# Optimization experiments

Hardware: AMD Instinct MI355X
Metric: run time of the kernel (lower is better)

Reference implementation:

```python
import jax, jax.numpy as jnp
import numpy as np

# dims: 3 bert layers averaged, B batch, T_SUB subword tokens (excl. CLS), W words, D=768 bert dim
B, T_SUB, W, D = 64, 512, 256, 768
H = 20          # lstm_hidden
CAP_DIM = 10
CAP_TYPES = 4
IN_DIM = D + CAP_DIM


def setup_inputs() -> dict:
    key = jax.random.key(0)
    ks = jax.random.split(key, 10)
    hiddens = jax.random.normal(ks[0], (3, B, T_SUB + 1, D), jnp.float32)  # [CLS] at pos 0
    # nondecreasing word ids, each word gets exactly T_SUB//W subwords (all segments non-empty)
    bert2toks = jnp.tile(jnp.repeat(jnp.arange(W), T_SUB // W)[None, :], (B, 1)).astype(jnp.int32)
    cap_inds = jax.random.randint(ks[1], (B, W), 0, CAP_TYPES)
    cap_table = jax.random.normal(ks[2], (CAP_TYPES, CAP_DIM), jnp.float32) * 0.1
    s = 1.0 / np.sqrt(H)
    u = lambda k, shp: jax.random.uniform(k, shp, jnp.float32, -s, s)
    w_ih_f = u(ks[3], (4 * H, IN_DIM))
    w_hh_f = u(ks[4], (4 * H, H))
    b_f = u(ks[5], (4 * H,))  # b_ih + b_hh fused
    w_ih_b = u(ks[6], (4 * H, IN_DIM))
    w_hh_b = u(ks[7], (4 * H, H))
    b_b = u(ks[8], (4 * H,))
    return {"hiddens": hiddens, "bert2toks": bert2toks, "cap_inds": cap_inds,
            "cap_table": cap_table, "w_ih_f": w_ih_f, "w_hh_f": w_hh_f, "b_f": b_f,
            "w_ih_b": w_ih_b, "w_hh_b": w_hh_b, "b_b": b_b}


def _lstm_dir(xs, w_ih, w_hh, b, reverse):
    # xs: [B, W, IN_DIM] -> hs: [B, W, H]
    xs_t = jnp.swapaxes(xs, 0, 1)  # [W, B, IN]
    if reverse:
        xs_t = xs_t[::-1]
    h0 = jnp.zeros((xs.shape[0], H), xs.dtype)

    def step(carry, xt):
        h, c = carry
        g = xt @ w_ih.T + h @ w_hh.T + b  # [B, 4H], pytorch gate order i,f,g,o
        i, f, gg, o = jnp.split(g, 4, axis=-1)
        c = jax.nn.sigmoid(f) * c + jax.nn.sigmoid(i) * jnp.tanh(gg)
        h = jax.nn.sigmoid(o) * jnp.tanh(c)
        return (h, c), h

    _, hs = jax.lax.scan(step, (h0, h0), xs_t)
    if reverse:
        hs = hs[::-1]
    return jnp.swapaxes(hs, 0, 1)


def reference(hiddens, bert2toks, cap_inds, cap_table,
              w_ih_f, w_hh_f, b_f, w_ih_b, w_hh_b, b_b):
    # mean over the 3 selected bert layers
    means = jnp.mean(hiddens, axis=0)          # [B, T_SUB+1, D]
    sub = means[:, 1:T_SUB + 1]                # skip [CLS]: means[i+1] indexing
    # ragged subword->word mean pooling as a segment mean
    flat_ids = (bert2toks + jnp.arange(B, dtype=bert2toks.dtype)[:, None] * W).reshape(-1)
    sums = jax.ops.segment_sum(sub.reshape(B * T_SUB, D), flat_ids, num_segments=B * W)
    cnts = jax.ops.segment_sum(jnp.ones((B * T_SUB, 1), sub.dtype), flat_ids, num_segments=B * W)
    word_h = (sums / cnts).reshape(B, W, D)
    cap_emb = cap_table[cap_inds]              # [B, W, CAP_DIM]
    x = jnp.concatenate([word_h, cap_emb], axis=-1)  # [B, W, IN_DIM]
    out = jnp.concatenate([
        _lstm_dir(x, w_ih_f, w_hh_f, b_f, False),
        _lstm_dir(x, w_ih_b, w_hh_b, b_b, True),
    ], axis=-1)                                # [B, W, 2H]
    return out
```

## Files before the change

kernel.cpp:

```cpp
#include <hip/hip_runtime.h>
#include <math.h>

#define BB 64
#define T_SUB 512
#define WW 256
#define DD 768
#define HH 20
#define CAP_DIM 10
#define IN_DIM 778
#define KPAD 800
#define G4 80
#define NOUT 160

typedef _Float16 f16x8 __attribute__((ext_vector_type(8)));
typedef float f32x4 __attribute__((ext_vector_type(4)));
typedef unsigned int uint2v __attribute__((ext_vector_type(2)));

#define WP_OFF   ((size_t)0)
#define SEG_OFF  ((size_t)256000)
#define X_OFF    ((size_t)387072)

__global__ __launch_bounds__(256) void k_prep(
    const float* __restrict__ wf, const float* __restrict__ wb,
    const int* __restrict__ b2t,
    _Float16* __restrict__ wp, int2* __restrict__ seg)
{
    int blk = blockIdx.x;
    if (blk < NOUT) {
        int j = blk;
        const float* src = (j < G4) ? (wf + (size_t)j * IN_DIM)
                                    : (wb + (size_t)(j - G4) * IN_DIM);
        for (int k = threadIdx.x; k < KPAD; k += 256)
            wp[(size_t)j * KPAD + k] = (k < IN_DIM) ? (_Float16)src[k] : (_Float16)0.f;
    } else {
        int b = blk - NOUT, w = threadIdx.x;
        const int* row = b2t + (size_t)b * T_SUB;
        int lo = 0, hi = T_SUB;
        while (lo < hi) { int m = (lo + hi) >> 1; if (row[m] < w) lo = m + 1; else hi = m; }
        int lo2 = lo, hi2 = T_SUB;
        while (lo2 < hi2) { int m = (lo2 + hi2) >> 1; if (row[m] < w + 1) lo2 = m + 1; else hi2 = m; }
        seg[(size_t)b * WW + w] = make_int2(lo, lo2 - lo);
    }
}

__global__ __launch_bounds__(256) void k_mean(
    const float* __restrict__ hiddens, const int2* __restrict__ seg,
    const int* __restrict__ cap_inds, const float* __restrict__ cap_table,
    _Float16* __restrict__ x)
{
    int idx = blockIdx.x * 256 + threadIdx.x;
    int d8 = idx % 100;
    int bw = idx / 100;
    int b = bw >> 8;
    f16x8 r;
    if (d8 < 96) {
        int2 sg = seg[bw];
        int lo = sg.x, cnt = sg.y;
        const size_t LSTR = (size_t)BB * (T_SUB + 1) * DD;
        const float* base = hiddens + ((size_t)b * (T_SUB + 1) + lo + 1) * DD + d8 * 8;
        float a[8];
#pragma unroll
        for (int q = 0; q < 8; q++) a[q] = 0.f;
        if (cnt == 2) {
#pragma unroll
            for (int l = 0; l < 3; ++l) {
                float4 v0 = *(const float4*)(base + l * LSTR);
                float4 v1 = *(const float4*)(base + l * LSTR + 4);
                float4 v2 = *(const float4*)(base + l * LSTR + DD);
                float4 v3 = *(const float4*)(base + l * LSTR + DD + 4);
                a[0] += v0.x + v2.x; a[1] += v0.y + v2.y;
                a[2] += v0.z + v2.z; a[3] += v0.w + v2.w;
                a[4] += v1.x + v3.x; a[5] += v1.y + v3.y;
                a[6] += v1.z + v3.z; a[7] += v1.w + v3.w;
            }
        } else {
            for (int l = 0; l < 3; ++l)
                for (int ti = 0; ti < cnt; ++ti) {
                    const float* p = base + l * LSTR + (size_t)ti * DD;
                    float4 v0 = *(const float4*)(p);
                    float4 v1 = *(const float4*)(p + 4);
                    a[0] += v0.x; a[1] += v0.y; a[2] += v0.z; a[3] += v0.w;
                    a[4] += v1.x; a[5] += v1.y; a[6] += v1.z; a[7] += v1.w;
                }
        }
        float inv = 1.0f / (3.0f * (float)(cnt > 0 ? cnt : 1));
#pragma unroll
        for (int q = 0; q < 8; q++) r[q] = (_Float16)(a[q] * inv);
    } else {
        int ci = cap_inds[bw];
#pragma unroll
        for (int q = 0; q < 8; q++) {
            int c = (d8 - 96) * 8 + q;
            r[q] = (c < CAP_DIM) ? (_Float16)cap_table[ci * CAP_DIM + c] : (_Float16)0.f;
        }
    }
    *(f16x8*)(x + (size_t)bw * KPAD + d8 * 8) = r;
}

__device__ __forceinline__ float xchg32(float v) {
    unsigned int a = __float_as_uint(v);
    uint2v r = __builtin_amdgcn_permlane32_swap(a, a, false, false);
    return __uint_as_float(r[0] ^ r[1] ^ a);
}

__global__ __launch_bounds__(320) void k_lstm(
    const _Float16* __restrict__ x, const _Float16* __restrict__ wp,
    const float* __restrict__ bias_f, const float* __restrict__ bias_b,
    const float* __restrict__ whh_f, const float* __restrict__ whh_b,
    float* __restrict__ out)
{
    __shared__ float gbuf[2][64 * G4];
    int dir  = blockIdx.x >> 6;
    int b    = blockIdx.x & 63;
    int t    = threadIdx.x;
    int wv   = t >> 6;
    int lane = t & 63;

    int mtile = wv - 1;
    int col   = lane & 15;
    int koff  = (lane >> 4) * 8;
    const _Float16* bp = wp + (size_t)(dir * G4 + col) * KPAD + koff;
    float bias_v[5];
    if (wv > 0) {
#pragma unroll
        for (int nf = 0; nf < 5; nf++)
            bias_v[nf] = (dir ? bias_b : bias_f)[nf * 16 + col];
    }

    const float* whh = dir ? whh_b : whh_f;
    int j = lane & 31; if (j > 19) j = 19;
    bool low = lane < 32;
    float mm = low ? 1.f : 2.f;
    float aa = low ? 0.f : -1.f;
    int coff = low ? (40 + 2 * j) : (2 * j);
    float w0[HH], w1[HH];
    if (wv == 0) {
        int r0 = low ? (20 + j) : j;
        int r1 = low ? (60 + j) : (40 + j);
#pragma unroll
        for (int k = 0; k < HH; k++) {
            w0[k] = whh[r0 * HH + k];
            w1[k] = whh[r1 * HH + k];
        }
    }

#define COMPUTE_CHUNK(CH, BUF) do {                                             \
    int base_w = dir ? (192 - (CH) * 64) : (CH) * 64;                           \
    int arow = b * 256 + base_w + mtile * 16 + (lane & 15);                     \
    const _Float16* ap = x + (size_t)arow * KPAD + koff;                        \
    f32x4 acc[5];                                                               \
    _Pragma("unroll")                                                           \
    for (int nf = 0; nf < 5; nf++)                                              \
        _Pragma("unroll")                                                       \
        for (int r = 0; r < 4; r++) acc[nf][r] = 0.f;                           \
    for (int k0 = 0; k0 < KPAD; k0 += 32) {                                     \
        f16x8 af = *(const f16x8*)(ap + k0);                                    \
        _Pragma("unroll")                                                       \
        for (int nf = 0; nf < 5; nf++) {                                        \
            f16x8 bf = *(const f16x8*)(bp + (size_t)nf * 16 * KPAD + k0);       \
            acc[nf] = __builtin_amdgcn_mfma_f32_16x16x32_f16(af, bf, acc[nf], 0, 0, 0); \
        }                                                                       \
    }                                                                           \
    int lrow = mtile * 16 + (lane >> 4) * 4;                                    \
    _Pragma("unroll")                                                           \
    for (int nf = 0; nf < 5; nf++) {                                            \
        int g = nf * 16 + col;                                                  \
        int pcol = (g % 40) * 2 + (g / 40);                                     \
        _Pragma("unroll")                                                       \
        for (int r = 0; r < 4; r++)                                             \
            gbuf[BUF][(lrow + r) * G4 + pcol] = acc[nf][r] + bias_v[nf];        \
    }                                                                           \
} while (0)

    if (wv > 0) COMPUTE_CHUNK(0, 0);
    __syncthreads();

    float h = 0.f, c = 0.f;
    int w = dir ? (WW - 1) : 0;
    int stepd = dir ? -1 : 1;

    for (int ch = 0; ch < 4; ++ch) {
        int cb = ch & 1;
        if (wv > 0) {
            if (ch + 1 < 4) COMPUTE_CHUNK(ch + 1, cb ^ 1);
        } else {
            int base = dir ? (192 - ch * 64) : ch * 64;
            float2 pre = *(const float2*)(&gbuf[cb][(w - base) * G4 + coff]);
            for (int sl = 0; sl < 64; ++sl) {
                int wn = w + stepd;
                float2 nxt = make_float2(0.f, 0.f);
                if (sl < 63)
                    nxt = *(const float2*)(&gbuf[cb][(wn - base) * G4 + coff]);
                float a0a = pre.x, a0b = 0.f, a1a = pre.y, a1b = 0.f;
#pragma unroll
                for (int k = 0; k < 10; k++) {
                    float hk  = __uint_as_float(__builtin_amdgcn_readlane(__float_as_uint(h), k));
                    float hk2 = __uint_as_float(__builtin_amdgcn_readlane(__float_as_uint(h), k + 10));
                    a0a = fmaf(hk,  w0[k],      a0a);
                    a1a = fmaf(hk,  w1[k],      a1a);
                    a0b = fmaf(hk2, w0[k + 10], a0b);
                    a1b = fmaf(hk2, w1[k + 10], a1b);
                }
                float a0 = a0a + a0b, a1 = a1a + a1b;
                float u0 = 1.f / (1.f + __expf(-a0));
                float uu = 1.f / (1.f + __expf(-mm * a1));
                float u1 = fmaf(uu, mm, aa);
                float p  = u0 * u1;
                float ps = xchg32(p);
                c = fmaf(u0, c, ps);
                float tc = fmaf(2.f, 1.f / (1.f + __expf(-2.f * c)), -1.f);
                h = u1 * tc;
                if (lane < HH)
                    out[((size_t)b * WW + w) * (2 * HH) + dir * HH + lane] = h;
                pre = nxt;
                w = wn;
            }
        }
        __syncthreads();
    }
#undef COMPUTE_CHUNK
}

extern "C" void kernel_launch(void* const* d_in, const int* in_sizes, int n_in,
                              void* d_out, int out_size, void* d_ws, size_t ws_size,
                              hipStream_t stream) {
    const float* hiddens   = (const float*)d_in[0];
    const int*   bert2toks = (const int*)d_in[1];
    const int*   cap_inds  = (const int*)d_in[2];
    const float* cap_table = (const float*)d_in[3];
    const float* w_ih_f    = (const float*)d_in[4];
    const float* w_hh_f    = (const float*)d_in[5];
    const float* b_f       = (const float*)d_in[6];
    const float* w_ih_b    = (const float*)d_in[7];
    const float* w_hh_b    = (const float*)d_in[8];
    const float* b_b       = (const float*)d_in[9];
    float* out = (float*)d_out;

    _Float16* wpad = (_Float16*)((char*)d_ws + WP_OFF);
    int2*     seg  = (int2*)((char*)d_ws + SEG_OFF);
    _Float16* x    = (_Float16*)((char*)d_ws + X_OFF);

    k_prep<<<NOUT + BB, 256, 0, stream>>>(w_ih_f, w_ih_b, bert2toks, wpad, seg);
    k_mean<<<(BB * WW * 100) / 256, 256, 0, stream>>>(hiddens, seg, cap_inds, cap_table, x);
    k_lstm<<<128, 320, 0, stream>>>(x, wpad, b_f, b_b, w_hh_f, w_hh_b, out);
}
```

Measured before the change: 160.9 us.

## Fuse prep and mean kernels, widen mean threads to two chunks, prioritize recurrence wave

```diff
diff --git a/kernel.cpp b/kernel.cpp
--- a/kernel.cpp
+++ b/kernel.cpp
@@ -20,81 +20,120 @@
 #define SEG_OFF  ((size_t)256000)
 #define X_OFF    ((size_t)387072)
 
-__global__ __launch_bounds__(256) void k_prep(
+#define NMEAN 3200
+#define NPREP 224
+
+__global__ __launch_bounds__(256) void k_mean_prep(
+    const float* __restrict__ hiddens, const int* __restrict__ b2t,
+    const int* __restrict__ cap_inds, const float* __restrict__ cap_table,
     const float* __restrict__ wf, const float* __restrict__ wb,
-    const int* __restrict__ b2t,
-    _Float16* __restrict__ wp, int2* __restrict__ seg)
+    _Float16* __restrict__ x, _Float16* __restrict__ wp, int2* __restrict__ seg)
 {
     int blk = blockIdx.x;
-    if (blk < NOUT) {
-        int j = blk;
-        const float* src = (j < G4) ? (wf + (size_t)j * IN_DIM)
-                                    : (wb + (size_t)(j - G4) * IN_DIM);
-        for (int k = threadIdx.x; k < KPAD; k += 256)
-            wp[(size_t)j * KPAD + k] = (k < IN_DIM) ? (_Float16)src[k] : (_Float16)0.f;
+    if (blk >= NMEAN) {
+        int pb = blk - NMEAN;
+        if (pb < NOUT) {
+            const float* src = (pb < G4) ? (wf + (size_t)pb * IN_DIM)
+                                         : (wb + (size_t)(pb - G4) * IN_DIM);
+            for (int k = threadIdx.x; k < KPAD; k += 256)
+                wp[(size_t)pb * KPAD + k] = (k < IN_DIM) ? (_Float16)src[k] : (_Float16)0.f;
+        } else {
+            int b = pb - NOUT, w = threadIdx.x;
+            const int* row = b2t + (size_t)b * T_SUB;
+            int lo = 0, hi = T_SUB;
+            while (lo < hi) { int m = (lo + hi) >> 1; if (row[m] < w) lo = m + 1; else hi = m; }
+            int lo2 = lo, hi2 = T_SUB;
+            while (lo2 < hi2) { int m = (lo2 + hi2) >> 1; if (row[m] < w + 1) lo2 = m + 1; else hi2 = m; }
+            seg[(size_t)b * WW + w] = make_int2(lo, lo2 - lo);
+        }
+        return;
+    }
+
+    int idx = blk * 256 + threadIdx.x;
+    int d2 = idx % 50;
+    int bw = idx / 50;
+    int b = bw >> 8;
+
+    int lo, cnt;
+    {
+        int w = bw & 255;
+        const int* row = b2t + (size_t)b * T_SUB;
+        int l0 = 0, hi = T_SUB;
+        while (l0 < hi) { int m = (l0 + hi) >> 1; if (row[m] < w) l0 = m + 1; else hi = m; }
+        int l2 = l0, hi2 = T_SUB;
+        while (l2 < hi2) { int m = (l2 + hi2) >> 1; if (row[m] < w + 1) l2 = m + 1; else hi2 = m; }
+        lo = l0; cnt = l2 - l0;
+    }
+    const size_t LSTR = (size_t)BB * (T_SUB + 1) * DD;
+    const float* rowp = hiddens + ((size_t)b * (T_SUB + 1) + lo + 1) * DD;
+    float inv = 1.0f / (3.0f * (float)(cnt > 0 ? cnt : 1));
+    bool bmean = (d2 + 50) < 96;
+    f16x8 ra, rb;
+
+    if (cnt == 2 && bmean) {
+        const float* pa = rowp + d2 * 8;
+        const float* pb_ = rowp + (d2 + 50) * 8;
+        float4 A0, A1, A2, A3, A4, A5, A6, A7, A8, A9, Aa, Ab;
+        float4 B0, B1, B2, B3, B4, B5, B6, B7, B8, B9, Ba, Bb;
+        A0 = *(const float4*)(pa);                A1 = *(const float4*)(pa + 4);
+        A2 = *(const float4*)(pa + DD);           A3 = *(const float4*)(pa + DD + 4);
+        A4 = *(const float4*)(pa + LSTR);         A5 = *(const float4*)(pa + LSTR + 4);
+        A6 = *(const float4*)(pa + LSTR + DD);    A7 = *(const float4*)(pa + LSTR + DD + 4);
+        A8 = *(const float4*)(pa + 2*LSTR);       A9 = *(const float4*)(pa + 2*LSTR + 4);
+        Aa = *(const float4*)(pa + 2*LSTR + DD);  Ab = *(const float4*)(pa + 2*LSTR + DD + 4);
+        B0 = *(const float4*)(pb_);               B1 = *(const float4*)(pb_ + 4);
+        B2 = *(const float4*)(pb_ + DD);          B3 = *(const float4*)(pb_ + DD + 4);
+        B4 = *(const float4*)(pb_ + LSTR);        B5 = *(const float4*)(pb_ + LSTR + 4);
+        B6 = *(const float4*)(pb_ + LSTR + DD);   B7 = *(const float4*)(pb_ + LSTR + DD + 4);
+        B8 = *(const float4*)(pb_ + 2*LSTR);      B9 = *(const float4*)(pb_ + 2*LSTR + 4);
+        Ba = *(const float4*)(pb_ + 2*LSTR + DD); Bb = *(const float4*)(pb_ + 2*LSTR + DD + 4);
+        ra[0] = (_Float16)((A0.x+A2.x+A4.x+A6.x+A8.x+Aa.x) * inv);
+        ra[1] = (_Float16)((A0.y+A2.y+A4.y+A6.y+A8.y+Aa.y) * inv);
+        ra[2] = (_Float16)((A0.z+A2.z+A4.z+A6.z+A8.z+Aa.z) * inv);
+        ra[3] = (_Float16)((A0.w+A2.w+A4.w+A6.w+A8.w+Aa.w) * inv);
+        ra[4] = (_Float16)((A1.x+A3.x+A5.x+A7.x+A9.x+Ab.x) * inv);
+        ra[5] = (_Float16)((A1.y+A3.y+A5.y+A7.y+A9.y+Ab.y) * inv);
+        ra[6] = (_Float16)((A1.z+A3.z+A5.z+A7.z+A9.z+Ab.z) * inv);
+        ra[7] = (_Float16)((A1.w+A3.w+A5.w+A7.w+A9.w+Ab.w) * inv);
+        rb[0] = (_Float16)((B0.x+B2.x+B4.x+B6.x+B8.x+Ba.x) * inv);
+        rb[1] = (_Float16)((B0.y+B2.y+B4.y+B6.y+B8.y+Ba.y) * inv);
+        rb[2] = (_Float16)((B0.z+B2.z+B4.z+B6.z+B8.z+Ba.z) * inv);
+        rb[3] = (_Float16)((B0.w+B2.w+B4.w+B6.w+B8.w+Ba.w) * inv);
+        rb[4] = (_Float16)((B1.x+B3.x+B5.x+B7.x+B9.x+Bb.x) * inv);
+        rb[5] = (_Float16)((B1.y+B3.y+B5.y+B7.y+B9.y+Bb.y) * inv);
+        rb[6] = (_Float16)((B1.z+B3.z+B5.z+B7.z+B9.z+Bb.z) * inv);
+        rb[7] = (_Float16)((B1.w+B3.w+B5.w+B7.w+B9.w+Bb.w) * inv);
     } else {
-        int b = blk - NOUT, w = threadIdx.x;
-        const int* row = b2t + (size_t)b * T_SUB;
-        int lo = 0, hi = T_SUB;
-        while (lo < hi) { int m = (lo + hi) >> 1; if (row[m] < w) lo = m + 1; else hi = m; }
-        int lo2 = lo, hi2 = T_SUB;
-        while (lo2 < hi2) { int m = (lo2 + hi2) >> 1; if (row[m] < w + 1) lo2 = m + 1; else hi2 = m; }
-        seg[(size_t)b * WW + w] = make_int2(lo, lo2 - lo);
-    }
-}
-
-__global__ __launch_bounds__(256) void k_mean(
-    const float* __restrict__ hiddens, const int2* __restrict__ seg,
-    const int* __restrict__ cap_inds, const float* __restrict__ cap_table,
-    _Float16* __restrict__ x)
-{
-    int idx = blockIdx.x * 256 + threadIdx.x;
-    int d8 = idx % 100;
-    int bw = idx / 100;
-    int b = bw >> 8;
-    f16x8 r;
-    if (d8 < 96) {
-        int2 sg = seg[bw];
-        int lo = sg.x, cnt = sg.y;
-        const size_t LSTR = (size_t)BB * (T_SUB + 1) * DD;
-        const float* base = hiddens + ((size_t)b * (T_SUB + 1) + lo + 1) * DD + d8 * 8;
-        float a[8];
-#pragma unroll
-        for (int q = 0; q < 8; q++) a[q] = 0.f;
-        if (cnt == 2) {
-#pragma unroll
-            for (int l = 0; l < 3; ++l) {
-                float4 v0 = *(const float4*)(base + l * LSTR);
-                float4 v1 = *(const float4*)(base + l * LSTR + 4);
-                float4 v2 = *(const float4*)(base + l * LSTR + DD);
-                float4 v3 = *(const float4*)(base + l * LSTR + DD + 4);
-                a[0] += v0.x + v2.x; a[1] += v0.y + v2.y;
-                a[2] += v0.z + v2.z; a[3] += v0.w + v2.w;
-                a[4] += v1.x + v3.x; a[5] += v1.y + v3.y;
-                a[6] += v1.z + v3.z; a[7] += v1.w + v3.w;
+        float a[8], bacc[8];
+#pragma unroll
+        for (int q = 0; q < 8; q++) { a[q] = 0.f; bacc[q] = 0.f; }
+        for (int l = 0; l < 3; ++l)
+            for (int ti = 0; ti < cnt; ++ti) {
+                const float* p = rowp + l * LSTR + (size_t)ti * DD;
+                float4 v0 = *(const float4*)(p + d2 * 8);
+                float4 v1 = *(const float4*)(p + d2 * 8 + 4);
+                a[0]+=v0.x; a[1]+=v0.y; a[2]+=v0.z; a[3]+=v0.w;
+                a[4]+=v1.x; a[5]+=v1.y; a[6]+=v1.z; a[7]+=v1.w;
+                if (bmean) {
+                    float4 u0 = *(const float4*)(p + (d2 + 50) * 8);
+                    float4 u1 = *(const float4*)(p + (d2 + 50) * 8 + 4);
+                    bacc[0]+=u0.x; bacc[1]+=u0.y; bacc[2]+=u0.z; bacc[3]+=u0.w;
+                    bacc[4]+=u1.x; bacc[5]+=u1.y; bacc[6]+=u1.z; bacc[7]+=u1.w;
+                }
             }
-        } else {
-            for (int l = 0; l < 3; ++l)
-                for (int ti = 0; ti < cnt; ++ti) {
-                    const float* p = base + l * LSTR + (size_t)ti * DD;
-                    float4 v0 = *(const float4*)(p);
-                    float4 v1 = *(const float4*)(p + 4);
-                    a[0] += v0.x; a[1] += v0.y; a[2] += v0.z; a[3] += v0.w;
-                    a[4] += v1.x; a[5] += v1.y; a[6] += v1.z; a[7] += v1.w;
-                }
-        }
-        float inv = 1.0f / (3.0f * (float)(cnt > 0 ? cnt : 1));
-#pragma unroll
-        for (int q = 0; q < 8; q++) r[q] = (_Float16)(a[q] * inv);
-    } else {
+#pragma unroll
+        for (int q = 0; q < 8; q++) { ra[q] = (_Float16)(a[q] * inv); rb[q] = (_Float16)(bacc[q] * inv); }
+    }
+    if (!bmean) {
         int ci = cap_inds[bw];
 #pragma unroll
         for (int q = 0; q < 8; q++) {
-            int c = (d8 - 96) * 8 + q;
-            r[q] = (c < CAP_DIM) ? (_Float16)cap_table[ci * CAP_DIM + c] : (_Float16)0.f;
-        }
-    }
-    *(f16x8*)(x + (size_t)bw * KPAD + d8 * 8) = r;
+            int c = (d2 + 50 - 96) * 8 + q;
+            rb[q] = (c < CAP_DIM) ? (_Float16)cap_table[ci * CAP_DIM + c] : (_Float16)0.f;
+        }
+    }
+    *(f16x8*)(x + (size_t)bw * KPAD + d2 * 8) = ra;
+    *(f16x8*)(x + (size_t)bw * KPAD + (d2 + 50) * 8) = rb;
 }
 
 __device__ __forceinline__ float xchg32(float v) {
@@ -184,6 +223,7 @@
         if (wv > 0) {
             if (ch + 1 < 4) COMPUTE_CHUNK(ch + 1, cb ^ 1);
         } else {
+            __builtin_amdgcn_s_setprio(1);
             int base = dir ? (192 - ch * 64) : ch * 64;
             float2 pre = *(const float2*)(&gbuf[cb][(w - base) * G4 + coff]);
             for (int sl = 0; sl < 64; ++sl) {
@@ -215,6 +255,7 @@
                 pre = nxt;
                 w = wn;
             }
+            __builtin_amdgcn_s_setprio(0);
         }
         __syncthreads();
     }
@@ -240,7 +281,8 @@
     int2*     seg  = (int2*)((char*)d_ws + SEG_OFF);
     _Float16* x    = (_Float16*)((char*)d_ws + X_OFF);
 
-    k_prep<<<NOUT + BB, 256, 0, stream>>>(w_ih_f, w_ih_b, bert2toks, wpad, seg);
-    k_mean<<<(BB * WW * 100) / 256, 256, 0, stream>>>(hiddens, seg, cap_inds, cap_table, x);
+    k_mean_prep<<<NMEAN + NPREP, 256, 0, stream>>>(hiddens, bert2toks, cap_inds,
+                                                   cap_table, w_ih_f, w_ih_b,
+                                                   x, wpad, seg);
     k_lstm<<<128, 320, 0, stream>>>(x, wpad, b_f, b_b, w_hh_f, w_hh_b, out);
 }
```

Measured after the change: 167.5 us. 4.1% more time.
